# Optimization experiments

Hardware: AMD Instinct MI355X
Metric: run time of the kernel (lower is better)

The kernel has to match this reference:

```python
import jax, jax.numpy as jnp
import numpy as np

LEAK = 0.2
NUM_GRAPHS = 64


def _gat(h_in, src, dst, eh, W, att_src, att_dst, att_edge, lin_edge_W, bias, N):
    # PyG GATConv with edge_dim, concat=False (mean over heads)
    H, C = att_src.shape
    h = (h_in @ W).reshape(N, H, C)                      # [N,H,C]
    e = (eh @ lin_edge_W).reshape(-1, H, C)              # [Eaug,H,C]
    a_s = jnp.einsum('nhc,hc->nh', h, att_src)           # [N,H]
    a_d = jnp.einsum('nhc,hc->nh', h, att_dst)
    a_e = jnp.einsum('ehc,hc->eh', e, att_edge)          # [Eaug,H]
    score = jax.nn.leaky_relu(a_s[src] + a_d[dst] + a_e, LEAK)
    # scatter-softmax over incoming edges of each destination node
    m = jax.ops.segment_max(score, dst, num_segments=N)
    ex = jnp.exp(score - m[dst])
    den = jax.ops.segment_sum(ex, dst, num_segments=N)
    alpha = ex / den[dst]                                # [Eaug,H]
    out = jax.ops.segment_sum(alpha[:, :, None] * h[src], dst, num_segments=N)
    return out.mean(axis=1) + bias                       # concat=False -> head mean


def setup_inputs() -> dict:
    key = jax.random.key(0)
    ks = jax.random.split(key, 32)
    N, E, F, FE, HID, H, NT = 30000, 480000, 64, 16, 64, 4, 16
    Cin1 = F + HID
    s = 0.05
    d = {
        'x': jax.random.normal(ks[0], (N, F), jnp.float32),
        'edge_attr': jax.random.normal(ks[1], (E, FE), jnp.float32),
        'node_emb': jax.random.normal(ks[2], (NT, HID), jnp.float32) * s,
        'edge_W': jax.random.normal(ks[3], (FE, HID), jnp.float32) * s,
        'edge_b': jnp.zeros((HID,), jnp.float32),
        'W1': jax.random.normal(ks[4], (Cin1, H * HID), jnp.float32) * s,
        'as1': jax.random.normal(ks[5], (H, HID), jnp.float32) * s,
        'ad1': jax.random.normal(ks[6], (H, HID), jnp.float32) * s,
        'ae1': jax.random.normal(ks[7], (H, HID), jnp.float32) * s,
        'leW1': jax.random.normal(ks[8], (HID, H * HID), jnp.float32) * s,
        'b1': jnp.zeros((HID,), jnp.float32),
        'W2': jax.random.normal(ks[9], (HID, H * HID), jnp.float32) * s,
        'as2': jax.random.normal(ks[10], (H, HID), jnp.float32) * s,
        'ad2': jax.random.normal(ks[11], (H, HID), jnp.float32) * s,
        'ae2': jax.random.normal(ks[12], (H, HID), jnp.float32) * s,
        'leW2': jax.random.normal(ks[13], (HID, H * HID), jnp.float32) * s,
        'b2': jnp.zeros((HID,), jnp.float32),
        'sage_Wl': jax.random.normal(ks[14], (HID, HID), jnp.float32) * s,
        'sage_bl': jnp.zeros((HID,), jnp.float32),
        'sage_Wr': jax.random.normal(ks[15], (HID, HID), jnp.float32) * s,
        'lin1_W': jax.random.normal(ks[16], (HID, HID), jnp.float32) * s,
        'lin1_b': jnp.zeros((HID,), jnp.float32),
        'lin2_W': jax.random.normal(ks[17], (HID, HID), jnp.float32) * s,
        'lin2_b': jnp.zeros((HID,), jnp.float32),
        'tel_W': jax.random.normal(ks[18], (HID, 1), jnp.float32) * s,
        'tel_b': jnp.zeros((1,), jnp.float32),
        'comp_W': jax.random.normal(ks[19], (HID, 1), jnp.float32) * s,
        'comp_b': jnp.zeros((1,), jnp.float32),
        'pch_W': jax.random.normal(ks[20], (HID, 1), jnp.float32) * s,
        'pch_b': jnp.zeros((1,), jnp.float32),
        'edge_index': jax.random.randint(ks[21], (2, E), 0, N, jnp.int32),
        'batch': jnp.sort(jax.random.randint(ks[22], (N,), 0, NUM_GRAPHS, jnp.int32)),
        'node_type': jax.random.randint(ks[23], (N,), 0, NT, jnp.int32),
    }
    return d


def reference(x, edge_attr, node_emb, edge_W, edge_b,
              W1, as1, ad1, ae1, leW1, b1,
              W2, as2, ad2, ae2, leW2, b2,
              sage_Wl, sage_bl, sage_Wr,
              lin1_W, lin1_b, lin2_W, lin2_b,
              tel_W, tel_b, comp_W, comp_b, pch_W, pch_b,
              edge_index, batch, node_type):
    N = x.shape[0]
    src0, dst0 = edge_index[0], edge_index[1]

    h0 = jnp.concatenate([x, node_emb[node_type]], axis=-1)   # [N, F+HID]
    eh = edge_attr @ edge_W + edge_b                          # [E, HID]

    # GATConv default add_self_loops=True, fill_value='mean' on edge_attr
    loop = jnp.arange(N, dtype=src0.dtype)
    src = jnp.concatenate([src0, loop])
    dst = jnp.concatenate([dst0, loop])
    eh_aug = jnp.concatenate([eh, jnp.broadcast_to(eh.mean(axis=0), (N, eh.shape[1]))], axis=0)

    h1 = jax.nn.elu(_gat(h0, src, dst, eh_aug, W1, as1, ad1, ae1, leW1, b1, N))
    h2 = jax.nn.elu(_gat(h1, src, dst, eh_aug, W2, as2, ad2, ae2, leW2, b2, N))

    # SAGEConv: mean neighbor aggregation (src->dst) + root transform
    deg = jax.ops.segment_sum(jnp.ones_like(dst0, dtype=h2.dtype), dst0, num_segments=N)
    agg = jax.ops.segment_sum(h2[src0], dst0, num_segments=N) / jnp.clip(deg, 1.0)[:, None]
    h3 = jax.nn.elu(agg @ sage_Wl + sage_bl + h2 @ sage_Wr)

    # global mean pool per graph
    cnt = jax.ops.segment_sum(jnp.ones((N,), h3.dtype), batch, num_segments=NUM_GRAPHS)
    g = jax.ops.segment_sum(h3, batch, num_segments=NUM_GRAPHS) / jnp.clip(cnt, 1.0)[:, None]

    g = jax.nn.elu(g @ lin1_W + lin1_b)                       # dropout inactive (eval)
    g = g @ lin2_W + lin2_b
    return (g @ tel_W + tel_b, g @ comp_W + comp_b, g @ pch_W + pch_b)
```

## Files before the change

### kernel.cpp

```cpp
#include <hip/hip_runtime.h>
#include <math.h>

#define NN 30000
#define NE 480000
#define FEA 16
#define HID 64
#define NG 64
#define LEAKK 0.2f

#define S_MEANEA 0
#define S_KF1    16
#define S_C1     80
#define S_AEL1   84
#define S_KF2    88
#define S_C2     152
#define S_AEL2   156
#define S_MS1    160
#define S_MD1    672
#define S_MS2    1184
#define S_MD2    1440

__device__ __forceinline__ float eluf(float v) { return v > 0.f ? v : expm1f(v); }
__device__ __forceinline__ float leakyf(float v) { return v >= 0.f ? v : LEAKK * v; }
__device__ __forceinline__ void fma4(float4& a, float w, const float4& x) {
    a.x += w * x.x; a.y += w * x.y; a.z += w * x.z; a.w += w * x.w;
}

__global__ __launch_bounds__(256) void count_mean_kernel(
    const int* __restrict__ dst, const float* __restrict__ EA,
    int* __restrict__ cnt, int* __restrict__ rank, float* __restrict__ S) {
    __shared__ float red[1024];
    int t = threadIdx.x;
    int base = blockIdx.x * 512;
#pragma unroll
    for (int i = 0; i < 2; i++) {
        int e = base + i * 256 + t;
        if (e < NE) rank[e] = atomicAdd(&cnt[dst[e]], 1);
    }
    int c4 = t & 3;
    int rbase = base + (t >> 2);
    float4 acc = {0, 0, 0, 0};
#pragma unroll
    for (int i = 0; i < 8; i++) {
        int r = rbase + i * 64;
        if (r < NE) {
            float4 v = *(const float4*)(EA + (size_t)r * FEA + c4 * 4);
            acc.x += v.x; acc.y += v.y; acc.z += v.z; acc.w += v.w;
        }
    }
    *(float4*)&red[t * 4] = acc;
    __syncthreads();
    if (t < 16) {
        int grp = t >> 2;
        int comp = t & 3;
        float sum = 0.f;
        for (int j = 0; j < 64; j++) sum += red[(grp + 4 * j) * 4 + comp];
        atomicAdd(&S[S_MEANEA + grp * 4 + comp], sum);
    }
}

__global__ void prep_all_kernel(
    const float* __restrict__ W1, const float* __restrict__ as1, const float* __restrict__ ad1,
    const float* __restrict__ ae1, const float* __restrict__ leW1,
    const float* __restrict__ W2, const float* __restrict__ as2, const float* __restrict__ ad2,
    const float* __restrict__ ae2, const float* __restrict__ leW2,
    const float* __restrict__ edge_W, const float* __restrict__ edge_b,
    const float* __restrict__ Wl, const float* __restrict__ Wr,
    const float* __restrict__ emb,
    float* __restrict__ S, float* __restrict__ WC1, float* __restrict__ WC2,
    float* __restrict__ B128) {
    int t = threadIdx.x;
    if (blockIdx.x > 0) {
        int i = (blockIdx.x - 1) * 256 + t;
        if (i < 16384) {
            int hk = i >> 6, c = i & 63;
            int h = hk >> 6, k = hk & 63;
            WC1[i] = 0.25f * W1[k * 256 + h * 64 + c];
        } else if (i < 20480) {
            int j2 = i - 16384;
            int r2 = j2 >> 6, c = j2 & 63;
            int h = r2 >> 4, tau = r2 & 15;
            float v = 0.f;
            for (int j = 0; j < 64; j++)
                v += emb[tau * 64 + j] * W1[(64 + j) * 256 + h * 64 + c];
            WC1[i] = 0.25f * v;
        } else if (i < 36864) {
            int j = i - 20480;
            int hk = j >> 6, c = j & 63;
            int h = hk >> 6, k = hk & 63;
            WC2[j] = 0.25f * W2[k * 256 + h * 64 + c];
        } else if (i < 45056) {
            int j = i - 36864;
            int k = j >> 6, c = j & 63;
            B128[j] = (k < 64) ? Wl[k * 64 + c] : Wr[(k - 64) * 64 + c];
        }
        return;
    }
    __shared__ float M1[256], M2[256], meh[64];
    if (t < 16) S[S_MEANEA + t] *= (1.0f / (float)NE);
    __syncthreads();
    {
        int k = t >> 2, h = t & 3;
        float m1 = 0.f, m2 = 0.f;
        for (int c = 0; c < 64; c++) {
            m1 += leW1[k * 256 + h * 64 + c] * ae1[h * 64 + c];
            m2 += leW2[k * 256 + h * 64 + c] * ae2[h * 64 + c];
        }
        M1[t] = m1; M2[t] = m2;
    }
    if (t < 64) {
        float v = edge_b[t];
        for (int f = 0; f < FEA; f++) v += S[S_MEANEA + f] * edge_W[f * 64 + t];
        meh[t] = v;
    }
    __syncthreads();
    if (t < 64) {
        int f = t >> 2, h = t & 3;
        float k1 = 0.f, k2 = 0.f;
        for (int k = 0; k < 64; k++) {
            k1 += edge_W[f * 64 + k] * M1[k * 4 + h];
            k2 += edge_W[f * 64 + k] * M2[k * 4 + h];
        }
        S[S_KF1 + t] = k1; S[S_KF2 + t] = k2;
    } else if (t < 68) {
        int h = t - 64;
        float c1 = 0.f, c2 = 0.f, a1 = 0.f, a2 = 0.f;
        for (int k = 0; k < 64; k++) {
            c1 += edge_b[k] * M1[k * 4 + h];
            c2 += edge_b[k] * M2[k * 4 + h];
            a1 += meh[k] * M1[k * 4 + h];
            a2 += meh[k] * M2[k * 4 + h];
        }
        S[S_C1 + h] = c1; S[S_C2 + h] = c2;
        S[S_AEL1 + h] = a1; S[S_AEL2 + h] = a2;
    }
    for (int i = t; i < 512; i += 256) {
        int k = i >> 2, h = i & 3;
        float s = 0.f, d = 0.f;
        for (int c = 0; c < 64; c++) {
            float w = W1[k * 256 + h * 64 + c];
            s += w * as1[h * 64 + c];
            d += w * ad1[h * 64 + c];
        }
        S[S_MS1 + i] = s; S[S_MD1 + i] = d;
    }
    for (int i = t; i < 256; i += 256) {
        int k = i >> 2, h = i & 3;
        float s = 0.f, d = 0.f;
        for (int c = 0; c < 64; c++) {
            float w = W2[k * 256 + h * 64 + c];
            s += w * as2[h * 64 + c];
            d += w * ad2[h * 64 + c];
        }
        S[S_MS2 + i] = s; S[S_MD2 + i] = d;
    }
}

__global__ __launch_bounds__(256) void attn_h0_kernel(
    const float* __restrict__ x, const float* __restrict__ node_emb,
    const int* __restrict__ node_type, const float* __restrict__ S,
    float* __restrict__ as_, float* __restrict__ ad_) {
    __shared__ float xt[64 * 132];
    __shared__ float ms[512], md[512];
    __shared__ int ntS[64];
    int t = threadIdx.x;
    int n0 = blockIdx.x * 64;
    if (t < 64) {
        int n = n0 + t;
        ntS[t] = (n < NN) ? node_type[n] : 0;
    }
    for (int i = t; i < 512; i += 256) { ms[i] = S[S_MS1 + i]; md[i] = S[S_MD1 + i]; }
    __syncthreads();
    for (int i = t; i < 1024; i += 256) {
        int r = i >> 4, c4 = (i & 15) * 4;
        int n = n0 + r;
        float4 f = {0, 0, 0, 0};
        if (n < NN) f = *(const float4*)(x + (size_t)n * 64 + c4);
        *(float4*)&xt[r * 132 + c4] = f;
    }
    for (int i = t; i < 1024; i += 256) {
        int r = i >> 4, c4 = (i & 15) * 4;
        int n = n0 + r;
        float4 f = {0, 0, 0, 0};
        if (n < NN) f = *(const float4*)(node_emb + (size_t)ntS[r] * 64 + c4);
        *(float4*)&xt[r * 132 + 64 + c4] = f;
    }
    __syncthreads();
    int r = t >> 2, h = t & 3;
    float s = 0.f, d = 0.f;
#pragma unroll 8
    for (int k = 0; k < 128; k++) {
        float xv = xt[r * 132 + k];
        s += xv * ms[k * 4 + h];
        d += xv * md[k * 4 + h];
    }
    int n = n0 + r;
    if (n < NN) { as_[n * 4 + h] = s; ad_[n * 4 + h] = d; }
}

__global__ void scan_blocks_kernel(const int* __restrict__ cnt, int* __restrict__ eoff,
                                   int* __restrict__ bsum) {
    __shared__ int wsum[16];
    int t = threadIdx.x;
    int i = blockIdx.x * 1024 + t;
    int v = (i < NN) ? cnt[i] : 0;
    int lane = t & 63;
    int incl = v;
#pragma unroll
    for (int ofs = 1; ofs < 64; ofs <<= 1) {
        int u = __shfl_up(incl, ofs, 64);
        if (lane >= ofs) incl += u;
    }
    int wid = t >> 6;
    if (lane == 63) wsum[wid] = incl;
    __syncthreads();
    if (t < 16) {
        int s = wsum[t];
#pragma unroll
        for (int ofs = 1; ofs < 16; ofs <<= 1) {
            int u = __shfl_up(s, ofs, 64);
            if (t >= ofs) s += u;
        }
        wsum[t] = s;
    }
    __syncthreads();
    int excl = incl - v + (wid > 0 ? wsum[wid - 1] : 0);
    if (i < NN) eoff[i] = excl;
    if (t == 1023) bsum[blockIdx.x] = excl + v;
}

__global__ void scan_tops_goff_kernel(const int* __restrict__ bsum, int* __restrict__ boff,
                                      int nb, const int* __restrict__ batch,
                                      int* __restrict__ goff) {
    int t = threadIdx.x;
    if (blockIdx.x == 1) {
        if (t > NG) return;
        int lo = 0, hi = NN;
        while (lo < hi) {
            int mid = (lo + hi) >> 1;
            if (batch[mid] < t) lo = mid + 1; else hi = mid;
        }
        goff[t] = lo;
        return;
    }
    if (t >= 64) return;
    int v = (t < nb) ? bsum[t] : 0;
    int incl = v;
#pragma unroll
    for (int ofs = 1; ofs < 64; ofs <<= 1) {
        int u = __shfl_up(incl, ofs, 64);
        if (t >= ofs) incl += u;
    }
    boff[t] = incl - v;
}

__global__ void scan_add_kernel(const int* __restrict__ boff, int* __restrict__ eoff) {
    int i = blockIdx.x * 256 + threadIdx.x;
    if (i < NN) eoff[i] += boff[i >> 10];
    if (i == 0) eoff[NN] = NE;
}

__global__ void scatter_score_kernel(const int* __restrict__ src, const int* __restrict__ dst,
                                     const float* __restrict__ EA, const float* __restrict__ S,
                                     const float* __restrict__ as_, const float* __restrict__ ad_,
                                     const int* __restrict__ node_type,
                                     const int* __restrict__ eoff, const int* __restrict__ rank,
                                     int2* __restrict__ se_sorted,
                                     float* __restrict__ sc1, float* __restrict__ ae2s) {
    int e = blockIdx.x * 256 + threadIdx.x;
    if (e >= NE) return;
    int s = src[e], d = dst[e];
    float a1[4], a2[4];
#pragma unroll
    for (int h = 0; h < 4; h++) { a1[h] = S[S_C1 + h]; a2[h] = S[S_C2 + h]; }
    const float4* EA4 = (const float4*)(EA + (size_t)e * FEA);
#pragma unroll
    for (int q = 0; q < 4; q++) {
        float4 v = EA4[q];
        float vv[4] = {v.x, v.y, v.z, v.w};
#pragma unroll
        for (int j = 0; j < 4; j++) {
            int f = q * 4 + j;
#pragma unroll
            for (int h = 0; h < 4; h++) {
                a1[h] += vv[j] * S[S_KF1 + f * 4 + h];
                a2[h] += vv[j] * S[S_KF2 + f * 4 + h];
            }
        }
    }
    ((float4*)ae2s)[e] = make_float4(a2[0], a2[1], a2[2], a2[3]);
    float4 asv = ((const float4*)as_)[s];
    float4 adv = ((const float4*)ad_)[d];
    float4 r;
    r.x = expf(leakyf(asv.x + adv.x + a1[0]));
    r.y = expf(leakyf(asv.y + adv.y + a1[1]));
    r.z = expf(leakyf(asv.z + adv.z + a1[2]));
    r.w = expf(leakyf(asv.w + adv.w + a1[3]));
    ((float4*)sc1)[e] = r;
    int ty = node_type[s];
    se_sorted[eoff[d] + rank[e]] = make_int2(s, e | (ty << 24));
}

__global__ void score2_kernel(const int* __restrict__ src, const int* __restrict__ dst,
                              const float* __restrict__ ae2s,
                              const float* __restrict__ as_, const float* __restrict__ ad_,
                              float* __restrict__ sc2) {
    int e = blockIdx.x * 256 + threadIdx.x;
    if (e >= NE) return;
    int s = src[e], d = dst[e];
    float4 ae = ((const float4*)ae2s)[e];
    float4 asv = ((const float4*)as_)[s];
    float4 adv = ((const float4*)ad_)[d];
    float4 r;
    r.x = expf(leakyf(asv.x + adv.x + ae.x));
    r.y = expf(leakyf(asv.y + adv.y + ae.y));
    r.z = expf(leakyf(asv.z + adv.z + ae.z));
    r.w = expf(leakyf(asv.w + adv.w + ae.w));
    ((float4*)sc2)[e] = r;
}

__global__ __launch_bounds__(256) void agg_gat1_kernel(
    const int* __restrict__ eoff, const int2* __restrict__ se_sorted,
    const float* __restrict__ sc1, const float* __restrict__ x,
    const int* __restrict__ node_type,
    const float* __restrict__ as_, const float* __restrict__ ad_,
    const float* __restrict__ Sael, float* __restrict__ agg) {
    int n = blockIdx.x * 4 + (threadIdx.x >> 6);
    if (n >= NN) return;
    int lane = threadIdx.x & 63;
    int sub = lane >> 4, ch = lane & 15;
    const float4* X4 = (const float4*)x;
    const float4* W4 = (const float4*)sc1;
    float4 asn = ((const float4*)as_)[n];
    float4 adn = ((const float4*)ad_)[n];
    float4 a0 = {0, 0, 0, 0}, a1 = a0, a2 = a0, a3 = a0, dn = a0, tw = a0;
    int b = eoff[n], e_end = eoff[n + 1];
    int nE = e_end - b;
    int i = sub;
    for (; i + 4 < nE; i += 8) {
        int2 se0 = se_sorted[b + i], se1 = se_sorted[b + i + 4];
        int e0 = se0.y & 0xFFFFFF, t0 = se0.y >> 24;
        int e1 = se1.y & 0xFFFFFF, t1 = se1.y >> 24;
        float4 w0 = W4[e0], w1 = W4[e1];
        float4 x0 = X4[(size_t)se0.x * 16 + ch];
        float4 x1 = X4[(size_t)se1.x * 16 + ch];
        fma4(a0, w0.x, x0); fma4(a1, w0.y, x0); fma4(a2, w0.z, x0); fma4(a3, w0.w, x0);
        fma4(a0, w1.x, x1); fma4(a1, w1.y, x1); fma4(a2, w1.z, x1); fma4(a3, w1.w, x1);
        dn.x += w0.x + w1.x; dn.y += w0.y + w1.y;
        dn.z += w0.z + w1.z; dn.w += w0.w + w1.w;
        if (ch == t0) { tw.x += w0.x; tw.y += w0.y; tw.z += w0.z; tw.w += w0.w; }
        if (ch == t1) { tw.x += w1.x; tw.y += w1.y; tw.z += w1.z; tw.w += w1.w; }
    }
    for (; i < nE; i += 4) {
        int2 se0 = se_sorted[b + i];
        int e0 = se0.y & 0xFFFFFF, t0 = se0.y >> 24;
        float4 w0 = W4[e0];
        float4 x0 = X4[(size_t)se0.x * 16 + ch];
        fma4(a0, w0.x, x0); fma4(a1, w0.y, x0); fma4(a2, w0.z, x0); fma4(a3, w0.w, x0);
        dn.x += w0.x; dn.y += w0.y; dn.z += w0.z; dn.w += w0.w;
        if (ch == t0) { tw.x += w0.x; tw.y += w0.y; tw.z += w0.z; tw.w += w0.w; }
    }
    if (sub == 0) {
        float e0 = expf(leakyf(asn.x + adn.x + Sael[0]));
        float e1 = expf(leakyf(asn.y + adn.y + Sael[1]));
        float e2 = expf(leakyf(asn.z + adn.z + Sael[2]));
        float e3 = expf(leakyf(asn.w + adn.w + Sael[3]));
        float4 xs = X4[(size_t)n * 16 + ch];
        fma4(a0, e0, xs); fma4(a1, e1, xs); fma4(a2, e2, xs); fma4(a3, e3, xs);
        dn.x += e0; dn.y += e1; dn.z += e2; dn.w += e3;
        int tn = node_type[n];
        if (ch == tn) { tw.x += e0; tw.y += e1; tw.z += e2; tw.w += e3; }
    }
#pragma unroll
    for (int mask = 16; mask < 64; mask <<= 1) {
        a0.x += __shfl_xor(a0.x, mask, 64); a0.y += __shfl_xor(a0.y, mask, 64);
        a0.z += __shfl_xor(a0.z, mask, 64); a0.w += __shfl_xor(a0.w, mask, 64);
        a1.x += __shfl_xor(a1.x, mask, 64); a1.y += __shfl_xor(a1.y, mask, 64);
        a1.z += __shfl_xor(a1.z, mask, 64); a1.w += __shfl_xor(a1.w, mask, 64);
        a2.x += __shfl_xor(a2.x, mask, 64); a2.y += __shfl_xor(a2.y, mask, 64);
        a2.z += __shfl_xor(a2.z, mask, 64); a2.w += __shfl_xor(a2.w, mask, 64);
        a3.x += __shfl_xor(a3.x, mask, 64); a3.y += __shfl_xor(a3.y, mask, 64);
        a3.z += __shfl_xor(a3.z, mask, 64); a3.w += __shfl_xor(a3.w, mask, 64);
        dn.x += __shfl_xor(dn.x, mask, 64); dn.y += __shfl_xor(dn.y, mask, 64);
        dn.z += __shfl_xor(dn.z, mask, 64); dn.w += __shfl_xor(dn.w, mask, 64);
        tw.x += __shfl_xor(tw.x, mask, 64); tw.y += __shfl_xor(tw.y, mask, 64);
        tw.z += __shfl_xor(tw.z, mask, 64); tw.w += __shfl_xor(tw.w, mask, 64);
    }
    if (sub == 0) {
        float i0 = 1.f / dn.x, i1 = 1.f / dn.y, i2 = 1.f / dn.z, i3 = 1.f / dn.w;
        float* A = agg + (size_t)n * 320;
        float4* A4 = (float4*)A;
        A4[ch]      = make_float4(a0.x * i0, a0.y * i0, a0.z * i0, a0.w * i0);
        A4[16 + ch] = make_float4(a1.x * i1, a1.y * i1, a1.z * i1, a1.w * i1);
        A4[32 + ch] = make_float4(a2.x * i2, a2.y * i2, a2.z * i2, a2.w * i2);
        A4[48 + ch] = make_float4(a3.x * i3, a3.y * i3, a3.z * i3, a3.w * i3);
        A[256 + ch]      = tw.x * i0;
        A[256 + 16 + ch] = tw.y * i1;
        A[256 + 32 + ch] = tw.z * i2;
        A[256 + 48 + ch] = tw.w * i3;
    }
}

__global__ __launch_bounds__(256) void agg_gat2_kernel(
    const int* __restrict__ eoff, const int2* __restrict__ se_sorted,
    const float* __restrict__ sc2, const float* __restrict__ X,
    const float* __restrict__ as_, const float* __restrict__ ad_,
    const float* __restrict__ Sael, float* __restrict__ agg) {
    int n = blockIdx.x * 4 + (threadIdx.x >> 6);
    if (n >= NN) return;
    int lane = threadIdx.x & 63;
    int sub = lane >> 4, ch = lane & 15;
    const float4* X4 = (const float4*)X;
    const float4* W4 = (const float4*)sc2;
    float4 asn = ((const float4*)as_)[n];
    float4 adn = ((const float4*)ad_)[n];
    float4 a0 = {0, 0, 0, 0}, a1 = a0, a2 = a0, a3 = a0, dn = a0;
    int b = eoff[n], e = eoff[n + 1];
    int nE = e - b;
    int i = sub;
    for (; i + 4 < nE; i += 8) {
        int2 se0 = se_sorted[b + i], se1 = se_sorted[b + i + 4];
        float4 w0 = W4[se0.y & 0xFFFFFF], w1 = W4[se1.y & 0xFFFFFF];
        float4 x0 = X4[(size_t)se0.x * 16 + ch];
        float4 x1 = X4[(size_t)se1.x * 16 + ch];
        fma4(a0, w0.x, x0); fma4(a1, w0.y, x0); fma4(a2, w0.z, x0); fma4(a3, w0.w, x0);
        fma4(a0, w1.x, x1); fma4(a1, w1.y, x1); fma4(a2, w1.z, x1); fma4(a3, w1.w, x1);
        dn.x += w0.x + w1.x; dn.y += w0.y + w1.y;
        dn.z += w0.z + w1.z; dn.w += w0.w + w1.w;
    }
    for (; i < nE; i += 4) {
        int2 se0 = se_sorted[b + i];
        float4 w0 = W4[se0.y & 0xFFFFFF];
        float4 x0 = X4[(size_t)se0.x * 16 + ch];
        fma4(a0, w0.x, x0); fma4(a1, w0.y, x0); fma4(a2, w0.z, x0); fma4(a3, w0.w, x0);
        dn.x += w0.x; dn.y += w0.y; dn.z += w0.z; dn.w += w0.w;
    }
    if (sub == 0) {
        float e0 = expf(leakyf(asn.x + adn.x + Sael[0]));
        float e1 = expf(leakyf(asn.y + adn.y + Sael[1]));
        float e2 = expf(leakyf(asn.z + adn.z + Sael[2]));
        float e3 = expf(leakyf(asn.w + adn.w + Sael[3]));
        float4 xs = X4[(size_t)n * 16 + ch];
        fma4(a0, e0, xs); fma4(a1, e1, xs); fma4(a2, e2, xs); fma4(a3, e3, xs);
        dn.x += e0; dn.y += e1; dn.z += e2; dn.w += e3;
    }
#pragma unroll
    for (int mask = 16; mask < 64; mask <<= 1) {
        a0.x += __shfl_xor(a0.x, mask, 64); a0.y += __shfl_xor(a0.y, mask, 64);
        a0.z += __shfl_xor(a0.z, mask, 64); a0.w += __shfl_xor(a0.w, mask, 64);
        a1.x += __shfl_xor(a1.x, mask, 64); a1.y += __shfl_xor(a1.y, mask, 64);
        a1.z += __shfl_xor(a1.z, mask, 64); a1.w += __shfl_xor(a1.w, mask, 64);
        a2.x += __shfl_xor(a2.x, mask, 64); a2.y += __shfl_xor(a2.y, mask, 64);
        a2.z += __shfl_xor(a2.z, mask, 64); a2.w += __shfl_xor(a2.w, mask, 64);
        a3.x += __shfl_xor(a3.x, mask, 64); a3.y += __shfl_xor(a3.y, mask, 64);
        a3.z += __shfl_xor(a3.z, mask, 64); a3.w += __shfl_xor(a3.w, mask, 64);
        dn.x += __shfl_xor(dn.x, mask, 64); dn.y += __shfl_xor(dn.y, mask, 64);
        dn.z += __shfl_xor(dn.z, mask, 64); dn.w += __shfl_xor(dn.w, mask, 64);
    }
    if (sub == 0) {
        float i0 = 1.f / dn.x, i1 = 1.f / dn.y, i2 = 1.f / dn.z, i3 = 1.f / dn.w;
        float4* agg4 = (float4*)(agg + (size_t)n * 256);
        agg4[ch]      = make_float4(a0.x * i0, a0.y * i0, a0.z * i0, a0.w * i0);
        agg4[16 + ch] = make_float4(a1.x * i1, a1.y * i1, a1.z * i1, a1.w * i1);
        agg4[32 + ch] = make_float4(a2.x * i2, a2.y * i2, a2.z * i2, a2.w * i2);
        agg4[48 + ch] = make_float4(a3.x * i3, a3.y * i3, a3.z * i3, a3.w * i3);
    }
}

template <int K, bool DOATT>
__global__ __launch_bounds__(256) void gemm64_kernel(
    const float* __restrict__ A, const float* __restrict__ B,
    const float* __restrict__ bias, float* __restrict__ out,
    const float* __restrict__ ms_g, const float* __restrict__ md_g,
    float* __restrict__ as_, float* __restrict__ ad_) {
    __shared__ float As[32 * 68];
    __shared__ float Bs[32 * 68];
    __shared__ float msS[256], mdS[256];
    int t = threadIdx.x;
    int tx = t & 15, ty = t >> 4;
    int m_base = blockIdx.x * 64;
    if (DOATT) { msS[t] = ms_g[t]; mdS[t] = md_g[t]; }
    int arow0 = t >> 3, akq0 = (t & 7) * 4;
    int arow1 = (t + 256) >> 3, akq1 = ((t + 256) & 7) * 4;
    int bkr = t >> 4, bnc = (t & 15) * 4;
    int am0 = m_base + arow0, am1 = m_base + arow1;
    float4 fa0, fa1, fb0, fb1;
    fa0 = (am0 < NN) ? *(const float4*)(A + (size_t)am0 * K + akq0) : make_float4(0, 0, 0, 0);
    fa1 = (am1 < NN) ? *(const float4*)(A + (size_t)am1 * K + akq1) : make_float4(0, 0, 0, 0);
    fb0 = *(const float4*)(B + (size_t)bkr * 64 + bnc);
    fb1 = *(const float4*)(B + (size_t)(bkr + 16) * 64 + bnc);
    float acc[4][4] = {};
    for (int k0 = 0;; k0 += 32) {
        As[(akq0 + 0) * 68 + arow0] = fa0.x;
        As[(akq0 + 1) * 68 + arow0] = fa0.y;
        As[(akq0 + 2) * 68 + arow0] = fa0.z;
        As[(akq0 + 3) * 68 + arow0] = fa0.w;
        As[(akq1 + 0) * 68 + arow1] = fa1.x;
        As[(akq1 + 1) * 68 + arow1] = fa1.y;
        As[(akq1 + 2) * 68 + arow1] = fa1.z;
        As[(akq1 + 3) * 68 + arow1] = fa1.w;
        *(float4*)&Bs[bkr * 68 + bnc] = fb0;
        *(float4*)&Bs[(bkr + 16) * 68 + bnc] = fb1;
        __syncthreads();
        bool more = (k0 + 32 < K);
        if (more) {
            int kn = k0 + 32;
            fa0 = (am0 < NN) ? *(const float4*)(A + (size_t)am0 * K + kn + akq0)
                             : make_float4(0, 0, 0, 0);
            fa1 = (am1 < NN) ? *(const float4*)(A + (size_t)am1 * K + kn + akq1)
                             : make_float4(0, 0, 0, 0);
            fb0 = *(const float4*)(B + (size_t)(kn + bkr) * 64 + bnc);
            fb1 = *(const float4*)(B + (size_t)(kn + bkr + 16) * 64 + bnc);
        }
#pragma unroll
        for (int k = 0; k < 32; k++) {
            float4 av = *(const float4*)&As[k * 68 + ty * 4];
            float4 bv = *(const float4*)&Bs[k * 68 + tx * 4];
            float a[4] = {av.x, av.y, av.z, av.w};
            float b[4] = {bv.x, bv.y, bv.z, bv.w};
#pragma unroll
            for (int i = 0; i < 4; i++)
#pragma unroll
                for (int j = 0; j < 4; j++) acc[i][j] += a[i] * b[j];
        }
        if (!more) break;
        __syncthreads();
    }
    float4 bvv = ((const float4*)bias)[tx];
    float o[4][4];
#pragma unroll
    for (int i = 0; i < 4; i++) {
        o[i][0] = eluf(acc[i][0] + bvv.x);
        o[i][1] = eluf(acc[i][1] + bvv.y);
        o[i][2] = eluf(acc[i][2] + bvv.z);
        o[i][3] = eluf(acc[i][3] + bvv.w);
        int m = m_base + ty * 4 + i;
        if (m < NN)
            *(float4*)(out + (size_t)m * 64 + tx * 4) =
                make_float4(o[i][0], o[i][1], o[i][2], o[i][3]);
    }
    if (DOATT) {
        float ps[4][4] = {}, pd[4][4] = {};
#pragma unroll
        for (int i = 0; i < 4; i++)
#pragma unroll
            for (int j = 0; j < 4; j++) {
                float v = o[i][j];
                int kk = (tx * 4 + j) * 4;
#pragma unroll
                for (int h = 0; h < 4; h++) {
                    ps[i][h] += v * msS[kk + h];
                    pd[i][h] += v * mdS[kk + h];
                }
            }
#pragma unroll
        for (int mk = 1; mk < 16; mk <<= 1) {
#pragma unroll
            for (int i = 0; i < 4; i++)
#pragma unroll
                for (int h = 0; h < 4; h++) {
                    ps[i][h] += __shfl_xor(ps[i][h], mk, 64);
                    pd[i][h] += __shfl_xor(pd[i][h], mk, 64);
                }
        }
        if (tx == 0) {
#pragma unroll
            for (int i = 0; i < 4; i++) {
                int m = m_base + ty * 4 + i;
                if (m < NN) {
                    *(float4*)(as_ + (size_t)m * 4) =
                        make_float4(ps[i][0], ps[i][1], ps[i][2], ps[i][3]);
                    *(float4*)(ad_ + (size_t)m * 4) =
                        make_float4(pd[i][0], pd[i][1], pd[i][2], pd[i][3]);
                }
            }
        }
    }
}

__global__ __launch_bounds__(256) void sage_agg3_kernel(
    const float* __restrict__ h2, const int* __restrict__ eoff,
    const int2* __restrict__ se_sorted, float* __restrict__ AB) {
    int n = blockIdx.x * 16 + (threadIdx.x >> 4);
    if (n >= NN) return;
    int l = threadIdx.x & 15;
    const float4* h24 = (const float4*)h2;
    float4* AB4 = (float4*)AB;
    float ax = 0.f, ay = 0.f, az = 0.f, aw = 0.f;
    int b = eoff[n], e_end = eoff[n + 1];
    int idx = b;
    int stop = b + ((e_end - b) & ~7);
    if (idx < stop) {
        int sreg[8];
#pragma unroll
        for (int u = 0; u < 8; u++) sreg[u] = se_sorted[idx + u].x;
        idx += 8;
        while (true) {
            int sn[8];
            bool more = idx < stop;
            if (more) {
#pragma unroll
                for (int u = 0; u < 8; u++) sn[u] = se_sorted[idx + u].x;
            }
#pragma unroll
            for (int u = 0; u < 8; u++) {
                float4 v = h24[(size_t)sreg[u] * 16 + l];
                ax += v.x; ay += v.y; az += v.z; aw += v.w;
            }
            if (!more) break;
#pragma unroll
            for (int u = 0; u < 8; u++) sreg[u] = sn[u];
            idx += 8;
        }
    }
    for (; idx < e_end; idx++) {
        float4 v0 = h24[(size_t)se_sorted[idx].x * 16 + l];
        ax += v0.x; ay += v0.y; az += v0.z; aw += v0.w;
    }
    float dg = (float)(e_end - b);
    if (dg < 1.f) dg = 1.f;
    float inv = 1.f / dg;
    AB4[(size_t)n * 32 + l] = make_float4(ax * inv, ay * inv, az * inv, aw * inv);
    AB4[(size_t)n * 32 + 16 + l] = h24[(size_t)n * 16 + l];
}

__global__ __launch_bounds__(256) void pool_mlp_kernel(
    const float* __restrict__ h3, const int* __restrict__ goff,
    const float* __restrict__ lin1W, const float* __restrict__ lin1b,
    const float* __restrict__ lin2W, const float* __restrict__ lin2b,
    const float* __restrict__ telW, const float* __restrict__ telb,
    const float* __restrict__ compW, const float* __restrict__ compb,
    const float* __restrict__ pchW, const float* __restrict__ pchb,
    float* __restrict__ out) {
    __shared__ float red[256];
    __shared__ float g[64], G1[64], G2[64];
    int gi = blockIdx.x, t = threadIdx.x;
    int c = t & 63, li = t >> 6;
    int b = goff[gi], e = goff[gi + 1];
    float sum = 0.f;
    for (int r = b + li; r < e; r += 4) sum += h3[(size_t)r * HID + c];
    red[t] = sum;
    __syncthreads();
    if (t < 64) {
        float v = red[t] + red[t + 64] + red[t + 128] + red[t + 192];
        float cntf = (float)(e - b);
        if (cntf < 1.f) cntf = 1.f;
        g[t] = v / cntf;
    }
    __syncthreads();
    {
        float part = 0.f;
#pragma unroll
        for (int k = li * 16; k < li * 16 + 16; k++) part += g[k] * lin1W[k * 64 + c];
        red[t] = part;
        __syncthreads();
        if (t < 64)
            G1[c] = eluf(red[c] + red[c + 64] + red[c + 128] + red[c + 192] + lin1b[c]);
        __syncthreads();
    }
    {
        float part = 0.f;
#pragma unroll
        for (int k = li * 16; k < li * 16 + 16; k++) part += G1[k] * lin2W[k * 64 + c];
        red[t] = part;
        __syncthreads();
        if (t < 64)
            G2[c] = red[c] + red[c + 64] + red[c + 128] + red[c + 192] + lin2b[c];
        __syncthreads();
    }
    if (t < 192) {
        int h = t >> 6, k = t & 63;
        const float* W = (h == 0) ? telW : ((h == 1) ? compW : pchW);
        red[t] = G2[k] * W[k];
    }
    __syncthreads();
    if (t < 3) {
        float acc = 0.f;
        for (int k = 0; k < 64; k++) acc += red[t * 64 + k];
        float bb = (t == 0) ? telb[0] : ((t == 1) ? compb[0] : pchb[0]);
        out[t * 64 + gi] = acc + bb;
    }
}

extern "C" void kernel_launch(void* const* d_in, const int* in_sizes, int n_in,
                              void* d_out, int out_size, void* d_ws, size_t ws_size,
                              hipStream_t stream) {
    const float* x        = (const float*)d_in[0];
    const float* EA       = (const float*)d_in[1];
    const float* node_emb = (const float*)d_in[2];
    const float* edge_W   = (const float*)d_in[3];
    const float* edge_b   = (const float*)d_in[4];
    const float* W1       = (const float*)d_in[5];
    const float* as1      = (const float*)d_in[6];
    const float* ad1      = (const float*)d_in[7];
    const float* ae1      = (const float*)d_in[8];
    const float* leW1     = (const float*)d_in[9];
    const float* b1       = (const float*)d_in[10];
    const float* W2       = (const float*)d_in[11];
    const float* as2      = (const float*)d_in[12];
    const float* ad2      = (const float*)d_in[13];
    const float* ae2      = (const float*)d_in[14];
    const float* leW2     = (const float*)d_in[15];
    const float* b2       = (const float*)d_in[16];
    const float* sage_Wl  = (const float*)d_in[17];
    const float* sage_bl  = (const float*)d_in[18];
    const float* sage_Wr  = (const float*)d_in[19];
    const float* lin1_W   = (const float*)d_in[20];
    const float* lin1_b   = (const float*)d_in[21];
    const float* lin2_W   = (const float*)d_in[22];
    const float* lin2_b   = (const float*)d_in[23];
    const float* tel_W    = (const float*)d_in[24];
    const float* tel_b    = (const float*)d_in[25];
    const float* comp_W   = (const float*)d_in[26];
    const float* comp_b   = (const float*)d_in[27];
    const float* pch_W    = (const float*)d_in[28];
    const float* pch_b    = (const float*)d_in[29];
    const int* edge_index = (const int*)d_in[30];
    const int* batch      = (const int*)d_in[31];
    const int* node_type  = (const int*)d_in[32];
    float* outp = (float*)d_out;

    const int* srcp = edge_index;
    const int* dstp = edge_index + NE;

    float* wf = (float*)d_ws;
    constexpr size_t OFF_H3    = 0;
    constexpr size_t OFF_AGG   = OFF_H3 + (size_t)NN * 64;
    constexpr size_t OFF_H1    = OFF_AGG + (size_t)NN * 512;
    constexpr size_t OFF_H2    = OFF_H1 + (size_t)NN * 64;
    constexpr size_t OFF_SC    = OFF_H2 + (size_t)NN * 64;
    constexpr size_t OFF_AE2   = OFF_SC + (size_t)NE * 4;
    constexpr size_t OFF_AS    = OFF_AE2 + (size_t)NE * 4;
    constexpr size_t OFF_AD    = OFF_AS + (size_t)NN * 4;
    constexpr size_t OFF_SMALL = OFF_AD + (size_t)NN * 4;
    constexpr size_t OFF_WC1   = OFF_SMALL + 4096;
    constexpr size_t OFF_WC2   = OFF_WC1 + 20480;
    constexpr size_t OFF_B128  = OFF_WC2 + 16384;
    constexpr size_t F_TOTAL   = OFF_B128 + 8192;

    int* wi         = (int*)(wf + F_TOTAL);
    int* cnt        = wi;
    int* rank       = wi + NN;
    int* eoff       = rank + NE;
    int2* se_sorted = (int2*)(eoff + (NN + 2));
    int* goff       = (int*)(se_sorted + NE);
    int* bsum       = goff + (NG + 1);
    int* boff       = bsum + 64;

    float* h3    = wf + OFF_H3;
    float* aggb  = wf + OFF_AGG;
    float* h1    = wf + OFF_H1;
    float* h2    = wf + OFF_H2;
    float* sc    = wf + OFF_SC;
    float* ae2s  = wf + OFF_AE2;
    float* as_   = wf + OFF_AS;
    float* ad_   = wf + OFF_AD;
    float* S     = wf + OFF_SMALL;
    float* WC1   = wf + OFF_WC1;
    float* WC2   = wf + OFF_WC2;
    float* B128  = wf + OFF_B128;
    float* AB    = wf + OFF_AGG;

    hipMemsetAsync(S + S_MEANEA, 0, 16 * sizeof(float), stream);
    hipMemsetAsync(cnt, 0, NN * sizeof(int), stream);

    count_mean_kernel<<<(NE + 511) / 512, 256, 0, stream>>>(dstp, EA, cnt, rank, S);
    prep_all_kernel<<<177, 256, 0, stream>>>(W1, as1, ad1, ae1, leW1,
                                             W2, as2, ad2, ae2, leW2,
                                             edge_W, edge_b, sage_Wl, sage_Wr, node_emb,
                                             S, WC1, WC2, B128);
    {
        int nb = (NN + 1023) / 1024;
        scan_blocks_kernel<<<nb, 1024, 0, stream>>>(cnt, eoff, bsum);
        scan_tops_goff_kernel<<<2, 128, 0, stream>>>(bsum, boff, nb, batch, goff);
        scan_add_kernel<<<(NN + 255) / 256, 256, 0, stream>>>(boff, eoff);
    }
    attn_h0_kernel<<<(NN + 63) / 64, 256, 0, stream>>>(x, node_emb, node_type, S, as_, ad_);
    scatter_score_kernel<<<(NE + 255) / 256, 256, 0, stream>>>(
        srcp, dstp, EA, S, as_, ad_, node_type, eoff, rank, se_sorted, sc, ae2s);

    agg_gat1_kernel<<<(NN + 3) / 4, 256, 0, stream>>>(
        eoff, se_sorted, sc, x, node_type, as_, ad_, S + S_AEL1, aggb);
    gemm64_kernel<320, true><<<(NN + 63) / 64, 256, 0, stream>>>(
        aggb, WC1, b1, h1, S + S_MS2, S + S_MD2, as_, ad_);

    score2_kernel<<<(NE + 255) / 256, 256, 0, stream>>>(srcp, dstp, ae2s, as_, ad_, sc);
    agg_gat2_kernel<<<(NN + 3) / 4, 256, 0, stream>>>(
        eoff, se_sorted, sc, h1, as_, ad_, S + S_AEL2, aggb);
    gemm64_kernel<256, false><<<(NN + 63) / 64, 256, 0, stream>>>(
        aggb, WC2, b2, h2, nullptr, nullptr, nullptr, nullptr);

    sage_agg3_kernel<<<(NN + 15) / 16, 256, 0, stream>>>(h2, eoff, se_sorted, AB);
    gemm64_kernel<128, false><<<(NN + 63) / 64, 256, 0, stream>>>(
        AB, B128, sage_bl, h3, nullptr, nullptr, nullptr, nullptr);

    pool_mlp_kernel<<<NG, 256, 0, stream>>>(h3, goff, lin1_W, lin1_b, lin2_W, lin2_b,
                                            tel_W, tel_b, comp_W, comp_b, pch_W, pch_b, outp);
}
```

Baseline: 421.5 us.

## Merge preprocessing kernels to cut launches and double-buffer GEMM shared tiles

The edge count/mean kernel is merged with the weight-folding part of prep into one launch. The block-offset scan, graph offsets and the attention-matrix prep now share a single launch, and the scan-add is fused into the node attention kernel. Together this removes several kernel launches from the serial chain. Separately, the GEMM kernel double-buffers its shared-memory tiles so each k-step needs one barrier instead of two, at the cost of twice the tile shared memory, which may lower occupancy.

Result: faster. 411.5 us (-2.4%).

```diff
diff --git a/kernel.cpp b/kernel.cpp
--- a/kernel.cpp
+++ b/kernel.cpp
@@ -26,52 +26,17 @@
     a.x += w * x.x; a.y += w * x.y; a.z += w * x.z; a.w += w * x.w;
 }
 
-__global__ __launch_bounds__(256) void count_mean_kernel(
+__global__ __launch_bounds__(256) void cm_prepw_kernel(
     const int* __restrict__ dst, const float* __restrict__ EA,
-    int* __restrict__ cnt, int* __restrict__ rank, float* __restrict__ S) {
+    int* __restrict__ cnt, int* __restrict__ rank, float* __restrict__ S,
+    const float* __restrict__ W1, const float* __restrict__ W2,
+    const float* __restrict__ Wl, const float* __restrict__ Wr,
+    const float* __restrict__ emb,
+    float* __restrict__ WC1, float* __restrict__ WC2, float* __restrict__ B128) {
     __shared__ float red[1024];
     int t = threadIdx.x;
-    int base = blockIdx.x * 512;
-#pragma unroll
-    for (int i = 0; i < 2; i++) {
-        int e = base + i * 256 + t;
-        if (e < NE) rank[e] = atomicAdd(&cnt[dst[e]], 1);
-    }
-    int c4 = t & 3;
-    int rbase = base + (t >> 2);
-    float4 acc = {0, 0, 0, 0};
-#pragma unroll
-    for (int i = 0; i < 8; i++) {
-        int r = rbase + i * 64;
-        if (r < NE) {
-            float4 v = *(const float4*)(EA + (size_t)r * FEA + c4 * 4);
-            acc.x += v.x; acc.y += v.y; acc.z += v.z; acc.w += v.w;
-        }
-    }
-    *(float4*)&red[t * 4] = acc;
-    __syncthreads();
-    if (t < 16) {
-        int grp = t >> 2;
-        int comp = t & 3;
-        float sum = 0.f;
-        for (int j = 0; j < 64; j++) sum += red[(grp + 4 * j) * 4 + comp];
-        atomicAdd(&S[S_MEANEA + grp * 4 + comp], sum);
-    }
-}
-
-__global__ void prep_all_kernel(
-    const float* __restrict__ W1, const float* __restrict__ as1, const float* __restrict__ ad1,
-    const float* __restrict__ ae1, const float* __restrict__ leW1,
-    const float* __restrict__ W2, const float* __restrict__ as2, const float* __restrict__ ad2,
-    const float* __restrict__ ae2, const float* __restrict__ leW2,
-    const float* __restrict__ edge_W, const float* __restrict__ edge_b,
-    const float* __restrict__ Wl, const float* __restrict__ Wr,
-    const float* __restrict__ emb,
-    float* __restrict__ S, float* __restrict__ WC1, float* __restrict__ WC2,
-    float* __restrict__ B128) {
-    int t = threadIdx.x;
-    if (blockIdx.x > 0) {
-        int i = (blockIdx.x - 1) * 256 + t;
+    if (blockIdx.x < 176) {
+        int i = blockIdx.x * 256 + t;
         if (i < 16384) {
             int hk = i >> 6, c = i & 63;
             int h = hk >> 6, k = hk & 63;
@@ -96,7 +61,98 @@
         }
         return;
     }
+    int base = (blockIdx.x - 176) * 512;
+#pragma unroll
+    for (int i = 0; i < 2; i++) {
+        int e = base + i * 256 + t;
+        if (e < NE) rank[e] = atomicAdd(&cnt[dst[e]], 1);
+    }
+    int c4 = t & 3;
+    int rbase = base + (t >> 2);
+    float4 acc = {0, 0, 0, 0};
+#pragma unroll
+    for (int i = 0; i < 8; i++) {
+        int r = rbase + i * 64;
+        if (r < NE) {
+            float4 v = *(const float4*)(EA + (size_t)r * FEA + c4 * 4);
+            acc.x += v.x; acc.y += v.y; acc.z += v.z; acc.w += v.w;
+        }
+    }
+    *(float4*)&red[t * 4] = acc;
+    __syncthreads();
+    if (t < 16) {
+        int grp = t >> 2;
+        int comp = t & 3;
+        float sum = 0.f;
+        for (int j = 0; j < 64; j++) sum += red[(grp + 4 * j) * 4 + comp];
+        atomicAdd(&S[S_MEANEA + grp * 4 + comp], sum);
+    }
+}
+
+__global__ void scan_blocks_kernel(const int* __restrict__ cnt, int* __restrict__ eoff,
+                                   int* __restrict__ bsum) {
+    __shared__ int wsum[16];
+    int t = threadIdx.x;
+    int i = blockIdx.x * 1024 + t;
+    int v = (i < NN) ? cnt[i] : 0;
+    int lane = t & 63;
+    int incl = v;
+#pragma unroll
+    for (int ofs = 1; ofs < 64; ofs <<= 1) {
+        int u = __shfl_up(incl, ofs, 64);
+        if (lane >= ofs) incl += u;
+    }
+    int wid = t >> 6;
+    if (lane == 63) wsum[wid] = incl;
+    __syncthreads();
+    if (t < 16) {
+        int s = wsum[t];
+#pragma unroll
+        for (int ofs = 1; ofs < 16; ofs <<= 1) {
+            int u = __shfl_up(s, ofs, 64);
+            if (t >= ofs) s += u;
+        }
+        wsum[t] = s;
+    }
+    __syncthreads();
+    int excl = incl - v + (wid > 0 ? wsum[wid - 1] : 0);
+    if (i < NN) eoff[i] = excl;
+    if (t == 1023) bsum[blockIdx.x] = excl + v;
+}
+
+__global__ void tops_goff_prep_kernel(
+    const int* __restrict__ bsum, int* __restrict__ boff, int nb,
+    const int* __restrict__ batch, int* __restrict__ goff,
+    const float* __restrict__ W1, const float* __restrict__ as1, const float* __restrict__ ad1,
+    const float* __restrict__ ae1, const float* __restrict__ leW1,
+    const float* __restrict__ W2, const float* __restrict__ as2, const float* __restrict__ ad2,
+    const float* __restrict__ ae2, const float* __restrict__ leW2,
+    const float* __restrict__ edge_W, const float* __restrict__ edge_b,
+    float* __restrict__ S) {
     __shared__ float M1[256], M2[256], meh[64];
+    int t = threadIdx.x;
+    if (blockIdx.x == 0) {
+        if (t >= 64) return;
+        int v = (t < nb) ? bsum[t] : 0;
+        int incl = v;
+#pragma unroll
+        for (int ofs = 1; ofs < 64; ofs <<= 1) {
+            int u = __shfl_up(incl, ofs, 64);
+            if (t >= ofs) incl += u;
+        }
+        boff[t] = incl - v;
+        return;
+    }
+    if (blockIdx.x == 1) {
+        if (t > NG) return;
+        int lo = 0, hi = NN;
+        while (lo < hi) {
+            int mid = (lo + hi) >> 1;
+            if (batch[mid] < t) lo = mid + 1; else hi = mid;
+        }
+        goff[t] = lo;
+        return;
+    }
     if (t < 16) S[S_MEANEA + t] *= (1.0f / (float)NE);
     __syncthreads();
     {
@@ -156,7 +212,8 @@
     }
 }
 
-__global__ __launch_bounds__(256) void attn_h0_kernel(
+__global__ __launch_bounds__(256) void scanadd_attn_kernel(
+    const int* __restrict__ boff, int* __restrict__ eoff,
     const float* __restrict__ x, const float* __restrict__ node_emb,
     const int* __restrict__ node_type, const float* __restrict__ S,
     float* __restrict__ as_, float* __restrict__ ad_) {
@@ -164,7 +221,13 @@
     __shared__ float ms[512], md[512];
     __shared__ int ntS[64];
     int t = threadIdx.x;
-    int n0 = blockIdx.x * 64;
+    if (blockIdx.x < 118) {
+        int i = blockIdx.x * 256 + t;
+        if (i < NN) eoff[i] += boff[i >> 10];
+        if (i == 0) eoff[NN] = NE;
+        return;
+    }
+    int n0 = (blockIdx.x - 118) * 64;
     if (t < 64) {
         int n = n0 + t;
         ntS[t] = (n < NN) ? node_type[n] : 0;
@@ -196,68 +259,6 @@
     }
     int n = n0 + r;
     if (n < NN) { as_[n * 4 + h] = s; ad_[n * 4 + h] = d; }
-}
-
-__global__ void scan_blocks_kernel(const int* __restrict__ cnt, int* __restrict__ eoff,
-                                   int* __restrict__ bsum) {
-    __shared__ int wsum[16];
-    int t = threadIdx.x;
-    int i = blockIdx.x * 1024 + t;
-    int v = (i < NN) ? cnt[i] : 0;
-    int lane = t & 63;
-    int incl = v;
-#pragma unroll
-    for (int ofs = 1; ofs < 64; ofs <<= 1) {
-        int u = __shfl_up(incl, ofs, 64);
-        if (lane >= ofs) incl += u;
-    }
-    int wid = t >> 6;
-    if (lane == 63) wsum[wid] = incl;
-    __syncthreads();
-    if (t < 16) {
-        int s = wsum[t];
-#pragma unroll
-        for (int ofs = 1; ofs < 16; ofs <<= 1) {
-            int u = __shfl_up(s, ofs, 64);
-            if (t >= ofs) s += u;
-        }
-        wsum[t] = s;
-    }
-    __syncthreads();
-    int excl = incl - v + (wid > 0 ? wsum[wid - 1] : 0);
-    if (i < NN) eoff[i] = excl;
-    if (t == 1023) bsum[blockIdx.x] = excl + v;
-}
-
-__global__ void scan_tops_goff_kernel(const int* __restrict__ bsum, int* __restrict__ boff,
-                                      int nb, const int* __restrict__ batch,
-                                      int* __restrict__ goff) {
-    int t = threadIdx.x;
-    if (blockIdx.x == 1) {
-        if (t > NG) return;
-        int lo = 0, hi = NN;
-        while (lo < hi) {
-            int mid = (lo + hi) >> 1;
-            if (batch[mid] < t) lo = mid + 1; else hi = mid;
-        }
-        goff[t] = lo;
-        return;
-    }
-    if (t >= 64) return;
-    int v = (t < nb) ? bsum[t] : 0;
-    int incl = v;
-#pragma unroll
-    for (int ofs = 1; ofs < 64; ofs <<= 1) {
-        int u = __shfl_up(incl, ofs, 64);
-        if (t >= ofs) incl += u;
-    }
-    boff[t] = incl - v;
-}
-
-__global__ void scan_add_kernel(const int* __restrict__ boff, int* __restrict__ eoff) {
-    int i = blockIdx.x * 256 + threadIdx.x;
-    if (i < NN) eoff[i] += boff[i >> 10];
-    if (i == 0) eoff[NN] = NE;
 }
 
 __global__ void scatter_score_kernel(const int* __restrict__ src, const int* __restrict__ dst,
@@ -473,8 +474,8 @@
     const float* __restrict__ bias, float* __restrict__ out,
     const float* __restrict__ ms_g, const float* __restrict__ md_g,
     float* __restrict__ as_, float* __restrict__ ad_) {
-    __shared__ float As[32 * 68];
-    __shared__ float Bs[32 * 68];
+    __shared__ float As[2][32 * 68];
+    __shared__ float Bs[2][32 * 68];
     __shared__ float msS[256], mdS[256];
     int t = threadIdx.x;
     int tx = t & 15, ty = t >> 4;
@@ -489,19 +490,20 @@
     fa1 = (am1 < NN) ? *(const float4*)(A + (size_t)am1 * K + akq1) : make_float4(0, 0, 0, 0);
     fb0 = *(const float4*)(B + (size_t)bkr * 64 + bnc);
     fb1 = *(const float4*)(B + (size_t)(bkr + 16) * 64 + bnc);
+    As[0][(akq0 + 0) * 68 + arow0] = fa0.x;
+    As[0][(akq0 + 1) * 68 + arow0] = fa0.y;
+    As[0][(akq0 + 2) * 68 + arow0] = fa0.z;
+    As[0][(akq0 + 3) * 68 + arow0] = fa0.w;
+    As[0][(akq1 + 0) * 68 + arow1] = fa1.x;
+    As[0][(akq1 + 1) * 68 + arow1] = fa1.y;
+    As[0][(akq1 + 2) * 68 + arow1] = fa1.z;
+    As[0][(akq1 + 3) * 68 + arow1] = fa1.w;
+    *(float4*)&Bs[0][bkr * 68 + bnc] = fb0;
+    *(float4*)&Bs[0][(bkr + 16) * 68 + bnc] = fb1;
+    __syncthreads();
     float acc[4][4] = {};
+    int cur = 0;
     for (int k0 = 0;; k0 += 32) {
-        As[(akq0 + 0) * 68 + arow0] = fa0.x;
-        As[(akq0 + 1) * 68 + arow0] = fa0.y;
-        As[(akq0 + 2) * 68 + arow0] = fa0.z;
-        As[(akq0 + 3) * 68 + arow0] = fa0.w;
-        As[(akq1 + 0) * 68 + arow1] = fa1.x;
-        As[(akq1 + 1) * 68 + arow1] = fa1.y;
-        As[(akq1 + 2) * 68 + arow1] = fa1.z;
-        As[(akq1 + 3) * 68 + arow1] = fa1.w;
-        *(float4*)&Bs[bkr * 68 + bnc] = fb0;
-        *(float4*)&Bs[(bkr + 16) * 68 + bnc] = fb1;
-        __syncthreads();
         bool more = (k0 + 32 < K);
         if (more) {
             int kn = k0 + 32;
@@ -514,8 +516,8 @@
         }
 #pragma unroll
         for (int k = 0; k < 32; k++) {
-            float4 av = *(const float4*)&As[k * 68 + ty * 4];
-            float4 bv = *(const float4*)&Bs[k * 68 + tx * 4];
+            float4 av = *(const float4*)&As[cur][k * 68 + ty * 4];
+            float4 bv = *(const float4*)&Bs[cur][k * 68 + tx * 4];
             float a[4] = {av.x, av.y, av.z, av.w};
             float b[4] = {bv.x, bv.y, bv.z, bv.w};
 #pragma unroll
@@ -524,7 +526,19 @@
                 for (int j = 0; j < 4; j++) acc[i][j] += a[i] * b[j];
         }
         if (!more) break;
+        int nxt = cur ^ 1;
+        As[nxt][(akq0 + 0) * 68 + arow0] = fa0.x;
+        As[nxt][(akq0 + 1) * 68 + arow0] = fa0.y;
+        As[nxt][(akq0 + 2) * 68 + arow0] = fa0.z;
+        As[nxt][(akq0 + 3) * 68 + arow0] = fa0.w;
+        As[nxt][(akq1 + 0) * 68 + arow1] = fa1.x;
+        As[nxt][(akq1 + 1) * 68 + arow1] = fa1.y;
+        As[nxt][(akq1 + 2) * 68 + arow1] = fa1.z;
+        As[nxt][(akq1 + 3) * 68 + arow1] = fa1.w;
+        *(float4*)&Bs[nxt][bkr * 68 + bnc] = fb0;
+        *(float4*)&Bs[nxt][(bkr + 16) * 68 + bnc] = fb1;
         __syncthreads();
+        cur = nxt;
     }
     float4 bvv = ((const float4*)bias)[tx];
     float o[4][4];
@@ -764,18 +778,17 @@
     hipMemsetAsync(S + S_MEANEA, 0, 16 * sizeof(float), stream);
     hipMemsetAsync(cnt, 0, NN * sizeof(int), stream);
 
-    count_mean_kernel<<<(NE + 511) / 512, 256, 0, stream>>>(dstp, EA, cnt, rank, S);
-    prep_all_kernel<<<177, 256, 0, stream>>>(W1, as1, ad1, ae1, leW1,
-                                             W2, as2, ad2, ae2, leW2,
-                                             edge_W, edge_b, sage_Wl, sage_Wr, node_emb,
-                                             S, WC1, WC2, B128);
+    cm_prepw_kernel<<<176 + (NE + 511) / 512, 256, 0, stream>>>(
+        dstp, EA, cnt, rank, S, W1, W2, sage_Wl, sage_Wr, node_emb, WC1, WC2, B128);
     {
         int nb = (NN + 1023) / 1024;
         scan_blocks_kernel<<<nb, 1024, 0, stream>>>(cnt, eoff, bsum);
-        scan_tops_goff_kernel<<<2, 128, 0, stream>>>(bsum, boff, nb, batch, goff);
-        scan_add_kernel<<<(NN + 255) / 256, 256, 0, stream>>>(boff, eoff);
-    }
-    attn_h0_kernel<<<(NN + 63) / 64, 256, 0, stream>>>(x, node_emb, node_type, S, as_, ad_);
+        tops_goff_prep_kernel<<<3, 256, 0, stream>>>(
+            bsum, boff, nb, batch, goff,
+            W1, as1, ad1, ae1, leW1, W2, as2, ad2, ae2, leW2, edge_W, edge_b, S);
+        scanadd_attn_kernel<<<118 + (NN + 63) / 64, 256, 0, stream>>>(
+            boff, eoff, x, node_emb, node_type, S, as_, ad_);
+    }
     scatter_score_kernel<<<(NE + 255) / 256, 256, 0, stream>>>(
         srcp, dstp, EA, S, as_, ad_, node_type, eoff, rank, se_sorted, sc, ae2s);
 
```
